# Optimization experiments

Hardware: AMD Instinct MI355X
Metric: run time of the kernel (lower is better)

The kernel has to match this reference:

```python
import jax, jax.numpy as jnp
import numpy as np

ITERS = 3
K = 64
C = 256


def setup_inputs() -> dict:
    key = jax.random.key(0)
    ks = jax.random.split(key, 6)
    N, H, W = 2, 60, 60
    cnn_feature = jax.random.normal(ks[0], (N, C, H, W), dtype=jnp.float32)
    points = jax.random.normal(ks[1], (N, 3, H, W), dtype=jnp.float32)
    # torch Linear params: weight (out, in), bias (out,)
    s1 = 1.0 / np.sqrt(C)
    s2 = 1.0 / np.sqrt(2 * C)
    mlp_w = jax.random.uniform(ks[2], (C, C), jnp.float32, -s1, s1)
    mlp_b = jax.random.uniform(ks[3], (C,), jnp.float32, -s1, s1)
    rnn_w = jax.random.uniform(ks[4], (C, 2 * C), jnp.float32, -s2, s2)
    rnn_b = jax.random.uniform(ks[5], (C,), jnp.float32, -s2, s2)
    return {"cnn_feature": cnn_feature, "points": points, "mlp_w": mlp_w,
            "mlp_b": mlp_b, "rnn_w": rnn_w, "rnn_b": rnn_b}


def reference(cnn_feature, points, mlp_w, mlp_b, rnn_w, rnn_b):
    N, Cc, H, W = cnn_feature.shape
    HW = H * W
    pts = points.reshape(N, 3, HW).transpose(0, 2, 1)  # (N, HW, 3)
    # pairwise Euclidean distances via Gram matrix
    r = jnp.einsum('nid,njd->nij', pts, pts)           # (N, HW, HW)
    sq = jnp.einsum('nid,nid->ni', pts, pts)           # (N, HW)
    D = jnp.sqrt(jnp.maximum(sq[:, :, None] + sq[:, None, :] - 2.0 * r, 0.0))
    _, idx = jax.lax.top_k(-D, K)                      # (N, HW, K) smallest distances

    h = cnn_feature.transpose(0, 2, 3, 1).reshape(N, HW, Cc)  # (N, HW, C)
    bidx = jnp.arange(N)[:, None, None]
    for _ in range(ITERS):
        nb = h[bidx, idx]                              # (N, HW, K, C) gather
        nb = jax.nn.relu(jnp.einsum('nskc,dc->nskd', nb, mlp_w) + mlp_b)
        message = nb.mean(axis=2)                      # (N, HW, C)
        nh = jnp.concatenate([h, message], axis=-1)    # (N, HW, 2C)
        h = jax.nn.relu(jnp.einsum('nsc,dc->nsd', nh, rnn_w) + rnn_b)
    h = h.reshape(N, H, W, Cc).transpose(0, 3, 1, 2)   # (N, C, H, W)
    return jnp.concatenate([cnn_feature, h], axis=1)   # (N, 2C, H, W)
```

## Files before the change

kernel.cpp:

```cpp
#include <hip/hip_runtime.h>
#include <stdint.h>

typedef unsigned int uint;
typedef unsigned long long ull;

#define HW 3600
#define CDIM 256
#define KNN 64
#define M_REAL 7200
#define PADM 7232
#define QPB 8

#define TKB 900
#define IHB 904
#define SUB 64

#define LDB2 136

using short8  = __attribute__((ext_vector_type(8))) short;
using floatx4 = __attribute__((ext_vector_type(4))) float;

__device__ inline unsigned short f2bf(float f) {
    uint u = __float_as_uint(f);
    uint r = u + 0x7FFFu + ((u >> 16) & 1u);
    return (unsigned short)(r >> 16);
}
__device__ inline float bf2f(unsigned short b) {
    return __uint_as_float(((uint)b) << 16);
}

#define WAVE_LDS_FENCE() asm volatile("s_waitcnt lgkmcnt(0)" ::: "memory")

__device__ inline void wave_select(uint* hist, uint* s_bin, uint* s_want,
                                   int lane, uint want) {
    uint h0 = hist[4 * lane + 0], h1 = hist[4 * lane + 1];
    uint h2 = hist[4 * lane + 2], h3 = hist[4 * lane + 3];
    hist[4 * lane + 0] = 0; hist[4 * lane + 1] = 0;
    hist[4 * lane + 2] = 0; hist[4 * lane + 3] = 0;
    uint c4 = h0 + h1 + h2 + h3;
    uint v = c4;
    #pragma unroll
    for (int off = 1; off < 64; off <<= 1) {
        uint o = __shfl_up(v, off, 64);
        if (lane >= off) v += o;
    }
    uint below = v - c4;
    if (below < want && want <= v) {
        uint b = 4 * lane, c = below;
        if (c + h0 < want) { c += h0; b = 4 * lane + 1;
            if (c + h1 < want) { c += h1; b = 4 * lane + 2;
                if (c + h2 < want) { c += h2; b = 4 * lane + 3; } } }
        *s_bin = b;
        *s_want = want - c;
    }
}

union MegaSmem {
    struct {
        float4 pts[HW];
        uint hist[QPB][256];
        uint s_bin[QPB], s_want[QPB], s_cnt[QPB];
    } tk;
    struct { float tile[2][32][33]; } ih;
};

__global__ __launch_bounds__(512) void mega_kernel(
    const float* __restrict__ points, int* __restrict__ idx_out,
    const float* __restrict__ cnn, unsigned short* __restrict__ NH,
    float* __restrict__ out,
    const float* __restrict__ mw, const float* __restrict__ rw,
    unsigned short* __restrict__ mo, unsigned short* __restrict__ ro) {
    __shared__ MegaSmem sm;
    const int blk = blockIdx.x;

    if (blk >= TKB + IHB) {
        int i0 = (blk - TKB - IHB) * 2048 + threadIdx.x * 4;
        float4 v = *(const float4*)&rw[i0];
        uint2 p;
        p.x = (uint)f2bf(v.x) | ((uint)f2bf(v.y) << 16);
        p.y = (uint)f2bf(v.z) | ((uint)f2bf(v.w) << 16);
        *(uint2*)&ro[i0] = p;
        if (i0 < 65536) {
            float4 m = *(const float4*)&mw[i0];
            p.x = (uint)f2bf(m.x) | ((uint)f2bf(m.y) << 16);
            p.y = (uint)f2bf(m.z) | ((uint)f2bf(m.w) << 16);
            *(uint2*)&mo[i0] = p;
        }
        return;
    }

    if (blk >= TKB) {
        const int b = blk - TKB;
        const int n = b / 452;
        const int r = b - n * 452;
        const int hw0 = (r % 113) * 32;
        const int c0 = (r / 113) * 64 + ((threadIdx.x >> 8) << 5);
        const int t8 = threadIdx.x & 255;
        const int tx = t8 & 31;
        const int ty = t8 >> 5;
        float (*tile)[33] = sm.ih.tile[threadIdx.x >> 8];
        const float* __restrict__ src = cnn + (size_t)n * CDIM * HW;
        #pragma unroll
        for (int rr = 0; rr < 4; ++rr) {
            int cc = ty + rr * 8;
            int hw = hw0 + tx;
            if (hw < HW) {
                float v = src[(size_t)(c0 + cc) * HW + hw];
                tile[cc][tx] = v;
                out[(size_t)n * (2 * CDIM * HW) + (size_t)(c0 + cc) * HW + hw] = v;
            }
        }
        __syncthreads();
        #pragma unroll
        for (int rr = 0; rr < 4; ++rr) {
            int hh = ty + rr * 8;
            int hw = hw0 + hh;
            if (hw < HW)
                NH[(size_t)(n * HW + hw) * 512 + c0 + tx] = f2bf(tile[tx][hh]);
        }
        return;
    }

    const int wv = threadIdx.x >> 6;
    const int lane = threadIdx.x & 63;
    const int q = blk * QPB + wv;
    const int n = (blk * QPB) / HW;
    const int i = q - n * HW;

    const float* __restrict__ px = points + (size_t)n * 3 * HW;
    const float* __restrict__ py = px + HW;
    const float* __restrict__ pz = py + HW;

    for (int j = threadIdx.x; j < HW; j += 512)
        sm.tk.pts[j] = make_float4(px[j], py[j], pz[j], 0.0f);
    sm.tk.hist[wv][4 * lane + 0] = 0; sm.tk.hist[wv][4 * lane + 1] = 0;
    sm.tk.hist[wv][4 * lane + 2] = 0; sm.tk.hist[wv][4 * lane + 3] = 0;
    if (lane == 0) sm.tk.s_cnt[wv] = 0;
    __syncthreads();

    float4 pq = sm.tk.pts[i];
    const float xi = pq.x, yi = pq.y, zi = pq.z;
    const float sqi = xi * xi + yi * yi + zi * zi;

    uint qp[29];
    #pragma unroll
    for (int s = 0; s < 57; ++s) {
        int j = (s << 6) + lane;
        uint q16 = 0xFFFFu;
        if (j < HW) {
            float4 p = sm.tk.pts[j];
            float d2 = fmaxf(sqi + (p.x * p.x + p.y * p.y + p.z * p.z)
                             - 2.0f * (xi * p.x + yi * p.y + zi * p.z), 0.0f);
            q16 = (uint)fminf(d2 * 1024.0f, 65535.0f);
        }
        if (s & 1) qp[s >> 1] |= q16 << 16; else qp[s >> 1] = q16;
    }
    #define Q16(s) ((qp[(s) >> 1] >> (((s) & 1) << 4)) & 0xFFFFu)

    #pragma unroll
    for (int s = 0; s < 57; ++s) {
        int j = (s << 6) + lane;
        if (j < HW) atomicAdd(&sm.tk.hist[wv][Q16(s) >> 8], 1u);
    }
    WAVE_LDS_FENCE();
    wave_select(&sm.tk.hist[wv][0], &sm.tk.s_bin[wv], &sm.tk.s_want[wv], lane, KNN);
    WAVE_LDS_FENCE();
    const uint qT8 = sm.tk.s_bin[wv];
    const uint want2 = sm.tk.s_want[wv];

    #pragma unroll
    for (int s = 0; s < 57; ++s) {
        int j = (s << 6) + lane;
        uint k = Q16(s);
        if (j < HW && (k >> 8) == qT8)
            atomicAdd(&sm.tk.hist[wv][k & 255u], 1u);
    }
    WAVE_LDS_FENCE();
    wave_select(&sm.tk.hist[wv][0], &sm.tk.s_bin[wv], &sm.tk.s_want[wv], lane, want2);
    WAVE_LDS_FENCE();
    const uint qT16 = (qT8 << 8) | sm.tk.s_bin[wv];
    const uint want3 = sm.tk.s_want[wv];

    #pragma unroll
    for (int s = 0; s < 57; ++s) {
        if (Q16(s) < qT16) {
            uint pos = atomicAdd(&sm.tk.s_cnt[wv], 1u);
            if (pos < KNN) idx_out[(size_t)q * KNN + pos] = (s << 6) + lane;
        }
    }

    ull cand[4] = {~0ULL, ~0ULL, ~0ULL, ~0ULL};
    int ncand = 0;
    #pragma unroll
    for (int s = 0; s < 57; ++s) {
        int j = (s << 6) + lane;
        if (j < HW && Q16(s) == qT16) {
            float4 p = sm.tk.pts[j];
            float d2 = fmaxf(sqi + (p.x * p.x + p.y * p.y + p.z * p.z)
                             - 2.0f * (xi * p.x + yi * p.y + zi * p.z), 0.0f);
            ull key = ((ull)__float_as_uint(d2) << 32) | (uint)j;
            if      (ncand == 0) cand[0] = key;
            else if (ncand == 1) cand[1] = key;
            else if (ncand == 2) cand[2] = key;
            else if (ncand == 3) cand[3] = key;
            ++ncand;
        }
    }
    const int base = KNN - (int)want3;
    if (__ballot(ncand > 4) == 0ULL) {
        for (int r = 0; r < (int)want3; ++r) {
            ull best = cand[0] < cand[1] ? cand[0] : cand[1];
            ull b23  = cand[2] < cand[3] ? cand[2] : cand[3];
            best = best < b23 ? best : b23;
            #pragma unroll
            for (int off = 1; off < 64; off <<= 1) {
                ull o = __shfl_xor(best, off, 64);
                if (o < best) best = o;
            }
            if (lane == 0) idx_out[(size_t)q * KNN + base + r] = (int)(uint)best;
            #pragma unroll
            for (int c = 0; c < 4; ++c)
                if (cand[c] == best) cand[c] = ~0ULL;
        }
    } else {
        ull used = 0ULL;
        for (int r = 0; r < (int)want3; ++r) {
            ull best = ~0ULL;
            #pragma unroll
            for (int s = 0; s < 57; ++s) {
                int j = (s << 6) + lane;
                if (j < HW && Q16(s) == qT16 && !((used >> s) & 1ULL)) {
                    float4 p = sm.tk.pts[j];
                    float d2 = fmaxf(sqi + (p.x * p.x + p.y * p.y + p.z * p.z)
                                     - 2.0f * (xi * p.x + yi * p.y + zi * p.z), 0.0f);
                    ull key = ((ull)__float_as_uint(d2) << 32) | (uint)j;
                    if (key < best) best = key;
                }
            }
            #pragma unroll
            for (int off = 1; off < 64; off <<= 1) {
                ull o = __shfl_xor(best, off, 64);
                if (o < best) best = o;
            }
            uint jw = (uint)best;
            if (lane == 0) idx_out[(size_t)q * KNN + base + r] = (int)jw;
            if ((int)(jw & 63u) == lane) used |= 1ULL << (jw >> 6);
        }
    }
    #undef Q16
}


__global__ __launch_bounds__(256) void gemm_dual(
    const unsigned short* __restrict__ NH,
    const unsigned short* __restrict__ mwb,
    const float* __restrict__ mbias,
    const unsigned short* __restrict__ rwb,
    const float* __restrict__ rbias,
    unsigned short* __restrict__ Tb,
    float* __restrict__ P) {
    __shared__ __align__(16) unsigned short As[64 * LDB2];
    __shared__ __align__(16) unsigned short Bs[64 * LDB2];
    const int v = blockIdx.x;
    const bool is_mlp = v < 452;
    const int g = is_mlp ? v : v - 452;
    const int m0 = (g % 113) * 64;
    const int n0 = (g / 113) * 64;
    const unsigned short* __restrict__ W = is_mlp ? mwb : rwb;
    const int ldw = is_mlp ? 256 : 512;

    const int tid = threadIdx.x;
    const int lane = tid & 63;
    const int w = tid >> 6;
    const int wm = (w & 1) * 32;
    const int wn = (w >> 1) * 32;
    const int l15 = lane & 15;
    const int qd = lane >> 4;

    floatx4 acc[2][2];
    #pragma unroll
    for (int a = 0; a < 2; ++a)
        #pragma unroll
        for (int b = 0; b < 2; ++b)
            acc[a][b] = (floatx4){0.f, 0.f, 0.f, 0.f};

    const int srow = tid >> 4;
    const int scol = (tid & 15) * 8;

    for (int kc = 0; kc < 256; kc += 128) {
        if (kc) __syncthreads();
        #pragma unroll
        for (int r4 = 0; r4 < 4; ++r4) {
            int row = r4 * 16 + srow;
            *(float4*)&As[row * LDB2 + scol] =
                *(const float4*)&NH[(size_t)(m0 + row) * 512 + kc + scol];
            *(float4*)&Bs[row * LDB2 + scol] =
                *(const float4*)&W[(size_t)(n0 + row) * ldw + kc + scol];
        }
        __syncthreads();
        #pragma unroll
        for (int ks = 0; ks < 128; ks += 32) {
            short8 a0 = *(const short8*)&As[(wm + l15) * LDB2 + ks + qd * 8];
            short8 a1 = *(const short8*)&As[(wm + 16 + l15) * LDB2 + ks + qd * 8];
            short8 b0 = *(const short8*)&Bs[(wn + l15) * LDB2 + ks + qd * 8];
            short8 b1 = *(const short8*)&Bs[(wn + 16 + l15) * LDB2 + ks + qd * 8];
            acc[0][0] = __builtin_amdgcn_mfma_f32_16x16x32_bf16(a0, b0, acc[0][0], 0, 0, 0);
            acc[0][1] = __builtin_amdgcn_mfma_f32_16x16x32_bf16(a0, b1, acc[0][1], 0, 0, 0);
            acc[1][0] = __builtin_amdgcn_mfma_f32_16x16x32_bf16(a1, b0, acc[1][0], 0, 0, 0);
            acc[1][1] = __builtin_amdgcn_mfma_f32_16x16x32_bf16(a1, b1, acc[1][1], 0, 0, 0);
        }
    }

    #pragma unroll
    for (int in = 0; in < 2; ++in) {
        int col = n0 + wn + in * 16 + l15;
        float bv = is_mlp ? mbias[col] : rbias[col];
        #pragma unroll
        for (int im = 0; im < 2; ++im) {
            int mb = m0 + wm + im * 16 + qd * 4;
            if (is_mlp) {
                #pragma unroll
                for (int r = 0; r < 4; ++r)
                    Tb[(size_t)(mb + r) * CDIM + col] =
                        f2bf(fmaxf(acc[im][in][r] + bv, 0.0f));
            } else {
                #pragma unroll
                for (int r = 0; r < 4; ++r)
                    P[(size_t)(mb + r) * CDIM + col] = acc[im][in][r] + bv;
            }
        }
    }
}

__global__ __launch_bounds__(256) void gemm_rnn2(
    const unsigned short* __restrict__ NH,
    const unsigned short* __restrict__ rwb,
    const float* __restrict__ P,
    unsigned short* __restrict__ Cb,
    float* __restrict__ outp, int mode) {
    __shared__ __align__(16) unsigned short As[64 * LDB2];
    __shared__ __align__(16) unsigned short Bs[64 * LDB2];
    const int m0 = (blockIdx.x % 113) * 64;
    const int n0 = (blockIdx.x / 113) * 64;

    const int tid = threadIdx.x;
    const int lane = tid & 63;
    const int w = tid >> 6;
    const int wm = (w & 1) * 32;
    const int wn = (w >> 1) * 32;
    const int l15 = lane & 15;
    const int qd = lane >> 4;

    floatx4 acc[2][2];
    #pragma unroll
    for (int a = 0; a < 2; ++a)
        #pragma unroll
        for (int b = 0; b < 2; ++b)
            acc[a][b] = (floatx4){0.f, 0.f, 0.f, 0.f};

    const int srow = tid >> 4;
    const int scol = (tid & 15) * 8;

    for (int kc = 0; kc < 256; kc += 128) {
        if (kc) __syncthreads();
        #pragma unroll
        for (int r4 = 0; r4 < 4; ++r4) {
            int row = r4 * 16 + srow;
            *(float4*)&As[row * LDB2 + scol] =
                *(const float4*)&NH[(size_t)(m0 + row) * 512 + 256 + kc + scol];
            *(float4*)&Bs[row * LDB2 + scol] =
                *(const float4*)&rwb[(size_t)(n0 + row) * 512 + 256 + kc + scol];
        }
        __syncthreads();
        #pragma unroll
        for (int ks = 0; ks < 128; ks += 32) {
            short8 a0 = *(const short8*)&As[(wm + l15) * LDB2 + ks + qd * 8];
            short8 a1 = *(const short8*)&As[(wm + 16 + l15) * LDB2 + ks + qd * 8];
            short8 b0 = *(const short8*)&Bs[(wn + l15) * LDB2 + ks + qd * 8];
            short8 b1 = *(const short8*)&Bs[(wn + 16 + l15) * LDB2 + ks + qd * 8];
            acc[0][0] = __builtin_amdgcn_mfma_f32_16x16x32_bf16(a0, b0, acc[0][0], 0, 0, 0);
            acc[0][1] = __builtin_amdgcn_mfma_f32_16x16x32_bf16(a0, b1, acc[0][1], 0, 0, 0);
            acc[1][0] = __builtin_amdgcn_mfma_f32_16x16x32_bf16(a1, b0, acc[1][0], 0, 0, 0);
            acc[1][1] = __builtin_amdgcn_mfma_f32_16x16x32_bf16(a1, b1, acc[1][1], 0, 0, 0);
        }
    }

    #pragma unroll
    for (int in = 0; in < 2; ++in) {
        int col = n0 + wn + in * 16 + l15;
        #pragma unroll
        for (int im = 0; im < 2; ++im) {
            int mb = m0 + wm + im * 16 + qd * 4;
            if (mode == 0) {
                #pragma unroll
                for (int r = 0; r < 4; ++r) {
                    float o = fmaxf(acc[im][in][r] + P[(size_t)(mb + r) * CDIM + col], 0.0f);
                    Cb[(size_t)(mb + r) * 512 + col] = f2bf(o);
                }
            } else if (mb < M_REAL) {
                int nb = mb / HW;
                int hw = mb - nb * HW;
                float4 o;
                o.x = fmaxf(acc[im][in][0] + P[(size_t)(mb + 0) * CDIM + col], 0.0f);
                o.y = fmaxf(acc[im][in][1] + P[(size_t)(mb + 1) * CDIM + col], 0.0f);
                o.z = fmaxf(acc[im][in][2] + P[(size_t)(mb + 2) * CDIM + col], 0.0f);
                o.w = fmaxf(acc[im][in][3] + P[(size_t)(mb + 3) * CDIM + col], 0.0f);
                *(float4*)&outp[(size_t)nb * (2 * CDIM * HW)
                                + (size_t)(CDIM + col) * HW + hw] = o;
            }
        }
    }
}

__global__ __launch_bounds__(256) void gather_mean(const unsigned short* __restrict__ T,
                                                   const int* __restrict__ idx,
                                                   unsigned short* __restrict__ NH) {
    const int q = blockIdx.x * 4 + (threadIdx.x >> 6);
    const int lane = threadIdx.x & 63;
    const int n = q / HW;
    const int half = lane >> 5;
    const int c8 = (lane & 31) * 8;

    const int nbrL = idx[(size_t)q * KNN + lane];
    float acc[8] = {0, 0, 0, 0, 0, 0, 0, 0};
    #pragma unroll 4
    for (int it = 0; it < 32; ++it) {
        int k = 2 * it + half;
        int j = __shfl(nbrL, k, 64);
        j = min(max(j, 0), HW - 1);
        int r = n * HW + j;
        uint4 v = *(const uint4*)&T[(size_t)r * CDIM + c8];
        acc[0] += bf2f((unsigned short)(v.x & 0xFFFFu));
        acc[1] += bf2f((unsigned short)(v.x >> 16));
        acc[2] += bf2f((unsigned short)(v.y & 0xFFFFu));
        acc[3] += bf2f((unsigned short)(v.y >> 16));
        acc[4] += bf2f((unsigned short)(v.z & 0xFFFFu));
        acc[5] += bf2f((unsigned short)(v.z >> 16));
        acc[6] += bf2f((unsigned short)(v.w & 0xFFFFu));
        acc[7] += bf2f((unsigned short)(v.w >> 16));
    }
    #pragma unroll
    for (int c = 0; c < 8; ++c) acc[c] += __shfl_xor(acc[c], 32, 64);
    if (half == 0) {
        uint4 o;
        o.x = (uint)f2bf(acc[0] * (1.0f / KNN)) | ((uint)f2bf(acc[1] * (1.0f / KNN)) << 16);
        o.y = (uint)f2bf(acc[2] * (1.0f / KNN)) | ((uint)f2bf(acc[3] * (1.0f / KNN)) << 16);
        o.z = (uint)f2bf(acc[4] * (1.0f / KNN)) | ((uint)f2bf(acc[5] * (1.0f / KNN)) << 16);
        o.w = (uint)f2bf(acc[6] * (1.0f / KNN)) | ((uint)f2bf(acc[7] * (1.0f / KNN)) << 16);
        *(uint4*)&NH[(size_t)q * 512 + CDIM + c8] = o;
    }
}

extern "C" void kernel_launch(void* const* d_in, const int* in_sizes, int n_in,
                              void* d_out, int out_size, void* d_ws, size_t ws_size,
                              hipStream_t stream) {
    const float* cnn   = (const float*)d_in[0];
    const float* pts   = (const float*)d_in[1];
    const float* mlp_w = (const float*)d_in[2];
    const float* mlp_b = (const float*)d_in[3];
    const float* rnn_w = (const float*)d_in[4];
    const float* rnn_b = (const float*)d_in[5];
    float* out = (float*)d_out;

    unsigned short* NHa    = (unsigned short*)d_ws;
    float*          P      = (float*)(NHa + (size_t)PADM * 512);
    unsigned short* Tb     = (unsigned short*)(P + (size_t)PADM * CDIM);
    unsigned short* mlpw_b = Tb + (size_t)PADM * CDIM;
    unsigned short* rnnw_b = mlpw_b + 65536;
    int*            idx    = (int*)(rnnw_b + 131072);

    mega_kernel<<<TKB + IHB + SUB, 512, 0, stream>>>(
        pts, idx, cnn, NHa, out, mlp_w, rnn_w, mlpw_b, rnnw_b);

    for (int it = 0; it < 3; ++it) {
        gemm_dual<<<904, 256, 0, stream>>>(
            NHa, mlpw_b, mlp_b, rnnw_b, rnn_b, Tb, P);
        gather_mean<<<M_REAL / 4, 256, 0, stream>>>(Tb, idx, NHa);
        if (it < 2) {
            gemm_rnn2<<<452, 256, 0, stream>>>(
                NHa, rnnw_b, P, NHa, nullptr, 0);
        } else {
            gemm_rnn2<<<452, 256, 0, stream>>>(
                NHa, rnnw_b, P, nullptr, out, 1);
        }
    }
}
```

Before: 209.9 us.

## Fuse neighbor gather-mean into the RNN message GEMM

Merges the gather_mean and gemm_rnn2 kernels into one gather_gemm kernel. Each block gathers and averages neighbours for 16 query rows straight into LDS, then multiplies them by the message half of the RNN weights, adding P and applying relu. This drops one launch per iteration and the write and re-read of the message half of NH through global memory. In exchange, each block reloads the full 256x256 weight slice and only 450 blocks run, each doing more serial gather work, which may lower parallelism.

```diff
diff --git a/kernel.cpp b/kernel.cpp
--- a/kernel.cpp
+++ b/kernel.cpp
@@ -16,6 +16,8 @@
 #define SUB 64
 
 #define LDB2 136
+#define LDG 264
+#define GGB 450
 
 using short8  = __attribute__((ext_vector_type(8))) short;
 using floatx4 = __attribute__((ext_vector_type(4))) float;
@@ -249,7 +251,6 @@
     }
     #undef Q16
 }
-
 
 __global__ __launch_bounds__(256) void gemm_dual(
     const unsigned short* __restrict__ NH,
@@ -332,122 +333,106 @@
     }
 }
 
-__global__ __launch_bounds__(256) void gemm_rnn2(
-    const unsigned short* __restrict__ NH,
+__global__ __launch_bounds__(256) void gather_gemm(
+    const unsigned short* __restrict__ T,
+    const int* __restrict__ idx,
+    const float* __restrict__ P,
     const unsigned short* __restrict__ rwb,
-    const float* __restrict__ P,
-    unsigned short* __restrict__ Cb,
+    unsigned short* __restrict__ NH,
     float* __restrict__ outp, int mode) {
-    __shared__ __align__(16) unsigned short As[64 * LDB2];
-    __shared__ __align__(16) unsigned short Bs[64 * LDB2];
-    const int m0 = (blockIdx.x % 113) * 64;
-    const int n0 = (blockIdx.x / 113) * 64;
-
+    __shared__ __align__(16) unsigned short As[16][LDG];
+    __shared__ __align__(16) unsigned short Bs[64][LDG];
+
+    const int m0 = blockIdx.x * 16;
     const int tid = threadIdx.x;
     const int lane = tid & 63;
-    const int w = tid >> 6;
-    const int wm = (w & 1) * 32;
-    const int wn = (w >> 1) * 32;
-    const int l15 = lane & 15;
-    const int qd = lane >> 4;
-
-    floatx4 acc[2][2];
-    #pragma unroll
-    for (int a = 0; a < 2; ++a)
-        #pragma unroll
-        for (int b = 0; b < 2; ++b)
-            acc[a][b] = (floatx4){0.f, 0.f, 0.f, 0.f};
-
-    const int srow = tid >> 4;
-    const int scol = (tid & 15) * 8;
-
-    for (int kc = 0; kc < 256; kc += 128) {
-        if (kc) __syncthreads();
-        #pragma unroll
-        for (int r4 = 0; r4 < 4; ++r4) {
-            int row = r4 * 16 + srow;
-            *(float4*)&As[row * LDB2 + scol] =
-                *(const float4*)&NH[(size_t)(m0 + row) * 512 + 256 + kc + scol];
-            *(float4*)&Bs[row * LDB2 + scol] =
-                *(const float4*)&rwb[(size_t)(n0 + row) * 512 + 256 + kc + scol];
-        }
-        __syncthreads();
-        #pragma unroll
-        for (int ks = 0; ks < 128; ks += 32) {
-            short8 a0 = *(const short8*)&As[(wm + l15) * LDB2 + ks + qd * 8];
-            short8 a1 = *(const short8*)&As[(wm + 16 + l15) * LDB2 + ks + qd * 8];
-            short8 b0 = *(const short8*)&Bs[(wn + l15) * LDB2 + ks + qd * 8];
-            short8 b1 = *(const short8*)&Bs[(wn + 16 + l15) * LDB2 + ks + qd * 8];
-            acc[0][0] = __builtin_amdgcn_mfma_f32_16x16x32_bf16(a0, b0, acc[0][0], 0, 0, 0);
-            acc[0][1] = __builtin_amdgcn_mfma_f32_16x16x32_bf16(a0, b1, acc[0][1], 0, 0, 0);
-            acc[1][0] = __builtin_amdgcn_mfma_f32_16x16x32_bf16(a1, b0, acc[1][0], 0, 0, 0);
-            acc[1][1] = __builtin_amdgcn_mfma_f32_16x16x32_bf16(a1, b1, acc[1][1], 0, 0, 0);
-        }
-    }
-
-    #pragma unroll
-    for (int in = 0; in < 2; ++in) {
-        int col = n0 + wn + in * 16 + l15;
-        #pragma unroll
-        for (int im = 0; im < 2; ++im) {
-            int mb = m0 + wm + im * 16 + qd * 4;
-            if (mode == 0) {
-                #pragma unroll
-                for (int r = 0; r < 4; ++r) {
-                    float o = fmaxf(acc[im][in][r] + P[(size_t)(mb + r) * CDIM + col], 0.0f);
-                    Cb[(size_t)(mb + r) * 512 + col] = f2bf(o);
-                }
-            } else if (mb < M_REAL) {
-                int nb = mb / HW;
-                int hw = mb - nb * HW;
-                float4 o;
-                o.x = fmaxf(acc[im][in][0] + P[(size_t)(mb + 0) * CDIM + col], 0.0f);
-                o.y = fmaxf(acc[im][in][1] + P[(size_t)(mb + 1) * CDIM + col], 0.0f);
-                o.z = fmaxf(acc[im][in][2] + P[(size_t)(mb + 2) * CDIM + col], 0.0f);
-                o.w = fmaxf(acc[im][in][3] + P[(size_t)(mb + 3) * CDIM + col], 0.0f);
-                *(float4*)&outp[(size_t)nb * (2 * CDIM * HW)
-                                + (size_t)(CDIM + col) * HW + hw] = o;
-            }
-        }
-    }
-}
-
-__global__ __launch_bounds__(256) void gather_mean(const unsigned short* __restrict__ T,
-                                                   const int* __restrict__ idx,
-                                                   unsigned short* __restrict__ NH) {
-    const int q = blockIdx.x * 4 + (threadIdx.x >> 6);
-    const int lane = threadIdx.x & 63;
-    const int n = q / HW;
+    const int wv = tid >> 6;
     const int half = lane >> 5;
     const int c8 = (lane & 31) * 8;
-
-    const int nbrL = idx[(size_t)q * KNN + lane];
-    float acc[8] = {0, 0, 0, 0, 0, 0, 0, 0};
+    const int n = m0 / HW;
+
+    int nbr[4];
+    #pragma unroll
+    for (int qi = 0; qi < 4; ++qi)
+        nbr[qi] = idx[(size_t)(m0 + wv * 4 + qi) * KNN + lane];
+    float acc[4][8];
+    #pragma unroll
+    for (int qi = 0; qi < 4; ++qi)
+        #pragma unroll
+        for (int c = 0; c < 8; ++c) acc[qi][c] = 0.0f;
+
     #pragma unroll 4
     for (int it = 0; it < 32; ++it) {
         int k = 2 * it + half;
-        int j = __shfl(nbrL, k, 64);
-        j = min(max(j, 0), HW - 1);
-        int r = n * HW + j;
-        uint4 v = *(const uint4*)&T[(size_t)r * CDIM + c8];
-        acc[0] += bf2f((unsigned short)(v.x & 0xFFFFu));
-        acc[1] += bf2f((unsigned short)(v.x >> 16));
-        acc[2] += bf2f((unsigned short)(v.y & 0xFFFFu));
-        acc[3] += bf2f((unsigned short)(v.y >> 16));
-        acc[4] += bf2f((unsigned short)(v.z & 0xFFFFu));
-        acc[5] += bf2f((unsigned short)(v.z >> 16));
-        acc[6] += bf2f((unsigned short)(v.w & 0xFFFFu));
-        acc[7] += bf2f((unsigned short)(v.w >> 16));
-    }
-    #pragma unroll
-    for (int c = 0; c < 8; ++c) acc[c] += __shfl_xor(acc[c], 32, 64);
-    if (half == 0) {
-        uint4 o;
-        o.x = (uint)f2bf(acc[0] * (1.0f / KNN)) | ((uint)f2bf(acc[1] * (1.0f / KNN)) << 16);
-        o.y = (uint)f2bf(acc[2] * (1.0f / KNN)) | ((uint)f2bf(acc[3] * (1.0f / KNN)) << 16);
-        o.z = (uint)f2bf(acc[4] * (1.0f / KNN)) | ((uint)f2bf(acc[5] * (1.0f / KNN)) << 16);
-        o.w = (uint)f2bf(acc[6] * (1.0f / KNN)) | ((uint)f2bf(acc[7] * (1.0f / KNN)) << 16);
-        *(uint4*)&NH[(size_t)q * 512 + CDIM + c8] = o;
+        #pragma unroll
+        for (int qi = 0; qi < 4; ++qi) {
+            int j = __shfl(nbr[qi], k, 64);
+            j = min(max(j, 0), HW - 1);
+            uint4 v = *(const uint4*)&T[(size_t)(n * HW + j) * CDIM + c8];
+            acc[qi][0] += bf2f((unsigned short)(v.x & 0xFFFFu));
+            acc[qi][1] += bf2f((unsigned short)(v.x >> 16));
+            acc[qi][2] += bf2f((unsigned short)(v.y & 0xFFFFu));
+            acc[qi][3] += bf2f((unsigned short)(v.y >> 16));
+            acc[qi][4] += bf2f((unsigned short)(v.z & 0xFFFFu));
+            acc[qi][5] += bf2f((unsigned short)(v.z >> 16));
+            acc[qi][6] += bf2f((unsigned short)(v.w & 0xFFFFu));
+            acc[qi][7] += bf2f((unsigned short)(v.w >> 16));
+        }
+    }
+    #pragma unroll
+    for (int qi = 0; qi < 4; ++qi) {
+        #pragma unroll
+        for (int c = 0; c < 8; ++c)
+            acc[qi][c] += __shfl_xor(acc[qi][c], 32, 64);
+        if (half == 0) {
+            uint4 o;
+            o.x = (uint)f2bf(acc[qi][0] * (1.0f / KNN)) | ((uint)f2bf(acc[qi][1] * (1.0f / KNN)) << 16);
+            o.y = (uint)f2bf(acc[qi][2] * (1.0f / KNN)) | ((uint)f2bf(acc[qi][3] * (1.0f / KNN)) << 16);
+            o.z = (uint)f2bf(acc[qi][4] * (1.0f / KNN)) | ((uint)f2bf(acc[qi][5] * (1.0f / KNN)) << 16);
+            o.w = (uint)f2bf(acc[qi][6] * (1.0f / KNN)) | ((uint)f2bf(acc[qi][7] * (1.0f / KNN)) << 16);
+            *(uint4*)&As[wv * 4 + qi][c8] = o;
+        }
+    }
+    __syncthreads();
+
+    const int l15 = lane & 15;
+    const int qd = lane >> 4;
+    const int brow = tid >> 2;
+    const int bseg = (tid & 3) * 64;
+    for (int nc = 0; nc < 4; ++nc) {
+        if (nc) __syncthreads();
+        const unsigned short* __restrict__ src =
+            &rwb[(size_t)(nc * 64 + brow) * 512 + 256 + bseg];
+        #pragma unroll
+        for (int u = 0; u < 8; ++u)
+            *(float4*)&Bs[brow][bseg + u * 8] = *(const float4*)&src[u * 8];
+        __syncthreads();
+
+        floatx4 o = (floatx4){0.f, 0.f, 0.f, 0.f};
+        #pragma unroll
+        for (int ks = 0; ks < 256; ks += 32) {
+            short8 a = *(const short8*)&As[l15][ks + qd * 8];
+            short8 b = *(const short8*)&Bs[wv * 16 + l15][ks + qd * 8];
+            o = __builtin_amdgcn_mfma_f32_16x16x32_bf16(a, b, o, 0, 0, 0);
+        }
+        const int col = nc * 64 + wv * 16 + l15;
+        const int mb = m0 + qd * 4;
+        if (mode == 0) {
+            #pragma unroll
+            for (int r = 0; r < 4; ++r) {
+                float hv = fmaxf(o[r] + P[(size_t)(mb + r) * CDIM + col], 0.0f);
+                NH[(size_t)(mb + r) * 512 + col] = f2bf(hv);
+            }
+        } else {
+            int hw = mb - n * HW;
+            float4 ov;
+            ov.x = fmaxf(o[0] + P[(size_t)(mb + 0) * CDIM + col], 0.0f);
+            ov.y = fmaxf(o[1] + P[(size_t)(mb + 1) * CDIM + col], 0.0f);
+            ov.z = fmaxf(o[2] + P[(size_t)(mb + 2) * CDIM + col], 0.0f);
+            ov.w = fmaxf(o[3] + P[(size_t)(mb + 3) * CDIM + col], 0.0f);
+            *(float4*)&outp[(size_t)n * (2 * CDIM * HW)
+                            + (size_t)(CDIM + col) * HW + hw] = ov;
+        }
     }
 }
 
@@ -475,13 +460,7 @@
     for (int it = 0; it < 3; ++it) {
         gemm_dual<<<904, 256, 0, stream>>>(
             NHa, mlpw_b, mlp_b, rnnw_b, rnn_b, Tb, P);
-        gather_mean<<<M_REAL / 4, 256, 0, stream>>>(Tb, idx, NHa);
-        if (it < 2) {
-            gemm_rnn2<<<452, 256, 0, stream>>>(
-                NHa, rnnw_b, P, NHa, nullptr, 0);
-        } else {
-            gemm_rnn2<<<452, 256, 0, stream>>>(
-                NHa, rnnw_b, P, nullptr, out, 1);
-        }
-    }
-}
+        gather_gemm<<<GGB, 256, 0, stream>>>(
+            Tb, idx, P, rnnw_b, NHa, out, it == 2 ? 1 : 0);
+    }
+}
```

After: 296.1 us. 41.1% more time.
